# Performance work log

Measured on AMD Instinct MI355X. Metric: run time of the kernel, lower is better.

The kernel has to match this reference:

```python
import jax, jax.numpy as jnp
import numpy as np

B, T, E, H, D, NL = 2, 1024, 2048, 16, 128, 3
MAXL = T * (2 ** (NL - 1))  # k length doubles each layer: T, 2T, 4T


def _rms_norm(x, w, eps=1e-5):
    return x * jax.lax.rsqrt(jnp.mean(x * x, axis=-1, keepdims=True) + eps) * w


def _rope(x, cos, sin):
    # x: [B, S, H, D]; cos/sin: [>=S, D/2]; GPT-NeoX style (non-interleaved)
    S = x.shape[1]
    c = cos[:S][None, :, None, :]
    s = sin[:S][None, :, None, :]
    x1, x2 = jnp.split(x, 2, axis=-1)
    return jnp.concatenate([x1 * c - x2 * s, x1 * s + x2 * c], axis=-1)


def _causal_attn(q, k, v):
    # bottom-right-aligned causal (flash_attn_func causal=True with kv longer than q)
    Tq, L = q.shape[1], k.shape[1]
    scale = 1.0 / np.sqrt(q.shape[-1]).astype(np.float32)
    scores = jnp.einsum('bthd,bshd->bhts', q, k) * scale
    i = jnp.arange(Tq)[:, None]
    j = jnp.arange(L)[None, :]
    mask = j <= i + (L - Tq)
    scores = jnp.where(mask[None, None], scores, -jnp.inf)
    p = jax.nn.softmax(scores, axis=-1)
    return jnp.einsum('bhts,bshd->bthd', p, v)


def setup_inputs() -> dict:
    key = jax.random.key(0)
    ks = jax.random.split(key, 6)
    x = jax.random.normal(ks[0], (B, T, E), dtype=jnp.float32)
    inv_freq = 1.0 / (10000.0 ** (np.arange(0, D, 2, dtype=np.float32) / D))  # [D/2]
    ang = np.arange(MAXL, dtype=np.float32)[:, None] * inv_freq[None, :]      # [MAXL, D/2]
    cos = jnp.asarray(np.cos(ang), dtype=jnp.float32)
    sin = jnp.asarray(np.sin(ang), dtype=jnp.float32)
    wq = jax.random.normal(ks[1], (NL, E, E), dtype=jnp.float32) * 0.02
    wk = jax.random.normal(ks[2], (NL, E, E), dtype=jnp.float32) * 0.02
    wv = jax.random.normal(ks[3], (NL, E, E), dtype=jnp.float32) * 0.02
    ln_w = jnp.ones((NL, E), dtype=jnp.float32)
    lambdas = jnp.zeros((NL,), dtype=jnp.float32)
    w_out = jax.random.normal(ks[4], (E, E), dtype=jnp.float32) * 0.02
    final_ln_w = jnp.ones((E,), dtype=jnp.float32)
    alpha = jnp.ones((1,), dtype=jnp.float32)
    return {'x': x, 'cos': cos, 'sin': sin, 'wq': wq, 'wk': wk, 'wv': wv,
            'ln_w': ln_w, 'lambdas': lambdas, 'w_out': w_out,
            'final_ln_w': final_ln_w, 'alpha': alpha}


def reference(x, cos, sin, wq, wk, wv, ln_w, lambdas, w_out, final_ln_w, alpha):
    bsz, tgt_len, embed_dim = x.shape
    # lambda weights: sigmoid then LayerNorm over the NL scalars (no affine)
    lam = jax.nn.sigmoid(lambdas)
    lam = (lam - jnp.mean(lam)) * jax.lax.rsqrt(jnp.var(lam) + 1e-5)
    acc_k, acc_v = [], []
    total = jnp.zeros_like(x)
    for i in range(NL):  # small fixed layer count
        q = (x @ wq[i].T).reshape(bsz, tgt_len, H, D)
        k = (x @ wk[i].T).reshape(bsz, tgt_len, H, D)
        v = (x @ wv[i].T).reshape(bsz, tgt_len, H, D)
        if i > 0:
            k = jnp.concatenate([k] + acc_k, axis=1)
            v = jnp.concatenate([v] + acc_v, axis=1)
        q = _rope(q, cos, sin)
        k = _rope(k, cos, sin)  # note: cached K gets rotary re-applied, as in source
        attn = _causal_attn(q, k, v).reshape(bsz, tgt_len, embed_dim)
        attn = _rms_norm(attn, ln_w[i])
        total = total + attn * lam[i]
        acc_k.append(k)
        acc_v.append(v)
    out = _rms_norm(total + alpha * x, final_ln_w)
    return out @ w_out.T
```

## Files before the change

kernel.cpp:

```cpp
#include <hip/hip_runtime.h>

typedef unsigned short ushort_t;
typedef __attribute__((ext_vector_type(8))) short bf16x8;
typedef __attribute__((ext_vector_type(4))) short bf16x4;
typedef __attribute__((ext_vector_type(4))) float f32x4;
typedef __attribute__((ext_vector_type(4))) unsigned short u16x4;
typedef __attribute__((ext_vector_type(4))) unsigned int u32x4;

#define DEV __device__ __forceinline__

DEV ushort_t f2bf(float f) {
  union { float f; unsigned int u; } a; a.f = f;
  unsigned int u = a.u;
  unsigned int r = (u + 0x7fffu + ((u >> 16) & 1u)) >> 16;
  return (ushort_t)r;
}
DEV float bf2f(ushort_t b) {
  union { float f; unsigned int u; } a; a.u = ((unsigned int)b) << 16;
  return a.f;
}
DEV void gload_lds16(const void* g, void* l) {
  __builtin_amdgcn_global_load_lds((const __attribute__((address_space(1))) void*)g,
                                   (__attribute__((address_space(3))) void*)l, 16, 0, 0);
}
DEV bf16x4 tr16(const ushort_t* l) {
  unsigned a = (unsigned)(unsigned long long)(const __attribute__((address_space(3))) ushort_t*)l;
  bf16x4 d;
  asm volatile("ds_read_b64_tr_b16 %0, %1" : "=v"(d) : "v"(a));
  return d;
}
DEV bf16x8 ldsb128(const ushort_t* l) {
  unsigned a = (unsigned)(unsigned long long)(const __attribute__((address_space(3))) ushort_t*)l;
  bf16x8 d;
  asm volatile("ds_read_b128 %0, %1" : "=v"(d) : "v"(a));
  return d;
}

__global__ __launch_bounds__(256) void f2b_kernel(const float* __restrict__ in,
                                                  ushort_t* __restrict__ out, int n) {
  int base = (blockIdx.x * 256 + threadIdx.x) * 4;
  if (base >= n) return;
  f32x4 v = *(const f32x4*)(in + base);
  u16x4 o;
  o.x = f2bf(v.x); o.y = f2bf(v.y); o.z = f2bf(v.z); o.w = f2bf(v.w);
  *(u16x4*)(out + base) = o;
}

__global__ __launch_bounds__(256) void f2b3_kernel(const float* __restrict__ a, const float* __restrict__ b,
                                                   const float* __restrict__ c, ushort_t* __restrict__ out) {
  int id = blockIdx.x * 256 + threadIdx.x;
  int sel = id >> 20, k = (id & 1048575) * 4;
  const float* src = sel == 0 ? a : sel == 1 ? b : c;
  f32x4 v = *(const f32x4*)(src + k);
  u16x4 o;
  o.x = f2bf(v.x); o.y = f2bf(v.y); o.z = f2bf(v.z); o.w = f2bf(v.w);
  *(u16x4*)(out + (size_t)sel * 4194304 + k) = o;
}

__global__ void lam_kernel(const float* __restrict__ lambdas, float* __restrict__ lam) {
  if (threadIdx.x == 0 && blockIdx.x == 0) {
    float l0 = 1.f / (1.f + __expf(-lambdas[0]));
    float l1 = 1.f / (1.f + __expf(-lambdas[1]));
    float l2 = 1.f / (1.f + __expf(-lambdas[2]));
    float mean = (l0 + l1 + l2) * (1.f / 3.f);
    float d0 = l0 - mean, d1 = l1 - mean, d2 = l2 - mean;
    float var = (d0 * d0 + d1 * d1 + d2 * d2) * (1.f / 3.f);
    float rs = rsqrtf(var + 1e-5f);
    lam[0] = d0 * rs; lam[1] = d1 * rs; lam[2] = d2 * rs;
  }
}

DEV void gemm_core(const ushort_t* __restrict__ A, const ushort_t* __restrict__ Bm,
                   ushort_t* lsA, ushort_t* lsB, int bm, int bn, f32x4 (&acc)[4][4]) {
  const int K = 2048;
  int tid = threadIdx.x;
  int w = tid >> 6, lane = tid & 63;
  int g = lane >> 4, r = lane & 15;
  int wm = w >> 1, wn = w & 1;
#pragma unroll
  for (int i = 0; i < 4; ++i)
#pragma unroll
    for (int j = 0; j < 4; ++j) acc[i][j] = 0.f;

  for (int kk = 0; kk < K; kk += 32) {
    __syncthreads();
#pragma unroll
    for (int j2 = 0; j2 < 2; ++j2) {
      int eb = w * 1024 + j2 * 512;
      int ebl = eb + lane * 8;
      int rr = ebl >> 5, cc = ebl & 31;
      gload_lds16(A + (size_t)(bm * 128 + rr) * K + kk + cc, lsA + eb);
      gload_lds16(Bm + (size_t)(bn * 128 + rr) * K + kk + cc, lsB + eb);
    }
    __syncthreads();
    bf16x8 af[4], bfr[4];
#pragma unroll
    for (int i = 0; i < 4; ++i)
      af[i] = *(const bf16x8*)(lsA + (wm * 64 + i * 16 + r) * 32 + g * 8);
#pragma unroll
    for (int j = 0; j < 4; ++j)
      bfr[j] = *(const bf16x8*)(lsB + (wn * 64 + j * 16 + r) * 32 + g * 8);
#pragma unroll
    for (int i = 0; i < 4; ++i)
#pragma unroll
      for (int j = 0; j < 4; ++j)
        acc[i][j] = __builtin_amdgcn_mfma_f32_16x16x32_bf16(af[i], bfr[j], acc[i][j], 0, 0, 0);
  }
}

__global__ __launch_bounds__(256) void gemm_qkv(
    const ushort_t* __restrict__ A,
    const ushort_t* __restrict__ Bq, const ushort_t* __restrict__ Bk, const ushort_t* __restrict__ Bv,
    ushort_t* __restrict__ Cq, ushort_t* __restrict__ Ck, ushort_t* __restrict__ Cv, int Lkv) {
  __shared__ __align__(16) ushort_t lsA[4096];
  __shared__ __align__(16) ushort_t lsB[4096];
  int sel = blockIdx.x >> 4, bn = blockIdx.x & 15, bm = blockIdx.y;
  const ushort_t* Bm = (sel == 0) ? Bq : (sel == 1) ? Bk : Bv;
  ushort_t* C = (sel == 0) ? Cq : (sel == 1) ? Ck : Cv;
  int Lsel = (sel == 0) ? 1024 : Lkv;
  f32x4 acc[4][4];
  gemm_core(A, Bm, lsA, lsB, bm, bn, acc);
  int lane = threadIdx.x & 63, w = threadIdx.x >> 6;
  int g = lane >> 4, r = lane & 15, wm = w >> 1, wn = w & 1;
#pragma unroll
  for (int i = 0; i < 4; ++i)
#pragma unroll
    for (int j = 0; j < 4; ++j) {
      int row0 = bm * 128 + wm * 64 + i * 16 + g * 4;
      int col = bn * 128 + wn * 64 + j * 16 + r;
#pragma unroll
      for (int t = 0; t < 4; ++t) {
        int row = row0 + t;
        int b2 = row >> 10, t2 = row & 1023;
        C[(size_t)(b2 * Lsel + t2) * 2048 + col] = f2bf(acc[i][j][t]);
      }
    }
}

__global__ __launch_bounds__(256) void gemm_bt_f32(
    const ushort_t* __restrict__ A, const ushort_t* __restrict__ Bm, float* __restrict__ C) {
  __shared__ __align__(16) ushort_t lsA[4096];
  __shared__ __align__(16) ushort_t lsB[4096];
  int bn = blockIdx.x, bm = blockIdx.y;
  f32x4 acc[4][4];
  gemm_core(A, Bm, lsA, lsB, bm, bn, acc);
  int lane = threadIdx.x & 63, w = threadIdx.x >> 6;
  int g = lane >> 4, r = lane & 15, wm = w >> 1, wn = w & 1;
#pragma unroll
  for (int i = 0; i < 4; ++i)
#pragma unroll
    for (int j = 0; j < 4; ++j) {
      int row0 = bm * 128 + wm * 64 + i * 16 + g * 4;
      int col = bn * 128 + wn * 64 + j * 16 + r;
#pragma unroll
      for (int t = 0; t < 4; ++t)
        C[(size_t)(row0 + t) * 2048 + col] = acc[i][j][t];
    }
}

__global__ __launch_bounds__(256) void rope_seg(const ushort_t* __restrict__ src, ushort_t* __restrict__ dst,
                                                const float* __restrict__ cosT, const float* __restrict__ sinT,
                                                int Ls, int s0, int Ld, int dpos0, int cnt) {
  int bp = blockIdx.x;
  int b = bp / cnt, pidx = bp % cnt;
  int pos = dpos0 + pidx;
  int pi = threadIdx.x * 4;
  int h = pi >> 6, d = pi & 63;
  const ushort_t* s_ = src + ((size_t)(b * Ls + s0 + pidx) * 16 + h) * 128 + d;
  ushort_t* d_ = dst + ((size_t)(b * Ld + pos) * 16 + h) * 128 + d;
  f32x4 c4 = *(const f32x4*)(cosT + (size_t)pos * 64 + d);
  f32x4 s4 = *(const f32x4*)(sinT + (size_t)pos * 64 + d);
  u16x4 x1 = *(const u16x4*)(s_);
  u16x4 x2 = *(const u16x4*)(s_ + 64);
  u16x4 o1, o2;
#pragma unroll
  for (int k = 0; k < 4; ++k) {
    float a = bf2f(x1[k]), bb = bf2f(x2[k]);
    o1[k] = f2bf(a * c4[k] - bb * s4[k]);
    o2[k] = f2bf(a * s4[k] + bb * c4[k]);
  }
  *(u16x4*)d_ = o1;
  *(u16x4*)(d_ + 64) = o2;
}

__global__ __launch_bounds__(256) void copy_seg(const ushort_t* __restrict__ src, ushort_t* __restrict__ dst,
                                                int Ls, int s0, int Ld, int dpos0, int cnt) {
  int bp = blockIdx.x;
  int b = bp / cnt, pidx = bp % cnt;
  const u32x4* s = (const u32x4*)(src + (size_t)(b * Ls + s0 + pidx) * 2048);
  u32x4* d = (u32x4*)(dst + (size_t)(b * Ld + dpos0 + pidx) * 2048);
  d[threadIdx.x] = s[threadIdx.x];
}

__global__ __launch_bounds__(256, 4) void attn_kernel(
    const ushort_t* __restrict__ Q, const ushort_t* __restrict__ Kc, const ushort_t* __restrict__ Vc,
    float* __restrict__ Opart, float2* __restrict__ Ml, int Lk) {
  __shared__ __align__(16) ushort_t lsK[8192];
  __shared__ __align__(16) ushort_t lsV[8192];
  const float sc = 0.08838834764831843f;

  int bid = (int)blockIdx.x;
  int swz = (bid & 7) * 128 + (bid >> 3);
  int s = swz & 1;
  int rest = swz >> 1;

  int w = threadIdx.x >> 6, lane = threadIdx.x & 63;
  int bq = rest & 15, h = (rest >> 4) & 15, b = rest >> 8;
  int qt = bq * 4 + w;
  int g = lane >> 4, r = lane & 15;
  int off = Lk - 1024;

  const ushort_t* qbase = Q + ((size_t)(b * 1024 + qt * 16 + r) * 16 + h) * 128;
  bf16x8 qf[4];
#pragma unroll
  for (int c = 0; c < 4; ++c) qf[c] = *(const bf16x8*)(qbase + c * 32 + g * 8);

  int t = threadIdx.x;
  int krow0 = t >> 4,        kc0 = (t & 15) ^ (krow0 & 7);
  int krow1 = (t + 256) >> 4, kc1 = (t & 15) ^ (krow1 & 7);
  const size_t adv = 32 * 2048;
  const size_t adv2 = 2 * adv;
  const ushort_t* srcK0 = Kc + ((size_t)(b * Lk + krow0) * 16 + h) * 128 + kc0 * 8 + s * adv;
  const ushort_t* srcK1 = Kc + ((size_t)(b * Lk + krow1) * 16 + h) * 128 + kc1 * 8 + s * adv;
  int L0 = t, L1 = t + 256;
  int vrow0 = ((L0 >> 3) & 7) * 4 + ((L0 >> 1) & 3), vd0 = (L0 >> 6) * 16 + (L0 & 1) * 8;
  int vrow1 = ((L1 >> 3) & 7) * 4 + ((L1 >> 1) & 3), vd1 = (L1 >> 6) * 16 + (L1 & 1) * 8;
  const ushort_t* srcV0 = Vc + ((size_t)(b * Lk + vrow0) * 16 + h) * 128 + vd0 + s * adv;
  const ushort_t* srcV1 = Vc + ((size_t)(b * Lk + vrow1) * 16 + h) * 128 + vd1 + s * adv;

  auto STAGE = [&](int buf) {
    ushort_t* k0 = lsK + buf * 4096 + w * 512;
    ushort_t* v0 = lsV + buf * 4096 + w * 512;
    gload_lds16(srcK0, k0);
    gload_lds16(srcK1, k0 + 2048);
    gload_lds16(srcV0, v0);
    gload_lds16(srcV1, v0 + 2048);
    srcK0 += adv2; srcK1 += adv2; srcV0 += adv2; srcV1 += adv2;
  };

  float m_run = -1e30f, l_run = 0.f;
  f32x4 o[8];
#pragma unroll
  for (int c = 0; c < 8; ++c) o[c] = 0.f;

  int qp = qt * 16 + r + off;
  int nkt_w = ((qt * 16 + 15 + off) >> 5) + 1;
  int nkt_blk = (((bq * 4 + 3) * 16 + 15 + off) >> 5) + 1;
  int ntile = (nkt_blk - s + 1) >> 1;

  if (ntile > 0) {
    STAGE(0);
    for (int it = 0; it < ntile; ++it) {
      int kt = s + it * 2;
      int cur = it & 1;
      if (it + 1 < ntile) {
        STAGE(cur ^ 1);
        asm volatile("s_waitcnt vmcnt(4)" ::: "memory");
      } else {
        asm volatile("s_waitcnt vmcnt(0)" ::: "memory");
      }
      __builtin_amdgcn_s_barrier();
      __builtin_amdgcn_sched_barrier(0);
      if (kt < nkt_w) {
        const ushort_t* Kb = lsK + cur * 4096;
        const ushort_t* Vb = lsV + cur * 4096;
        f32x4 st[2];
#pragma unroll
        for (int ks = 0; ks < 2; ++ks) {
          bf16x8 kf[4];
#pragma unroll
          for (int c = 0; c < 4; ++c)
            kf[c] = ldsb128(Kb + (ks * 16 + r) * 128 + ((c * 32 + g * 8) ^ ((r & 7) * 8)));
          asm volatile("s_waitcnt lgkmcnt(0)" ::: "memory");
          __builtin_amdgcn_sched_barrier(0);
          __builtin_amdgcn_s_setprio(1);
          f32x4 acc = 0.f;
#pragma unroll
          for (int c = 0; c < 4; ++c)
            acc = __builtin_amdgcn_mfma_f32_16x16x32_bf16(kf[c], qf[c], acc, 0, 0, 0);
          __builtin_amdgcn_s_setprio(0);
          st[ks] = acc;
        }
        float pmax = -1e30f;
        int kp0 = kt * 32;
#pragma unroll
        for (int ks = 0; ks < 2; ++ks)
#pragma unroll
          for (int j = 0; j < 4; ++j) {
            int key = kp0 + ks * 16 + g * 4 + j;
            float sv = st[ks][j] * sc;
            if (key > qp) sv = -1e30f;
            st[ks][j] = sv;
            pmax = fmaxf(pmax, sv);
          }
        pmax = fmaxf(pmax, __shfl_xor(pmax, 16, 64));
        pmax = fmaxf(pmax, __shfl_xor(pmax, 32, 64));
        if (!__all(pmax <= m_run + 8.f)) {
          float mnew = fmaxf(m_run, pmax);
          float corr = __expf(m_run - mnew);
          l_run *= corr;
#pragma unroll
          for (int c = 0; c < 8; ++c)
#pragma unroll
            for (int tt = 0; tt < 4; ++tt) o[c][tt] *= corr;
          m_run = mnew;
        }
        float psum = 0.f;
        bf16x4 pf[2];
#pragma unroll
        for (int ks = 0; ks < 2; ++ks)
#pragma unroll
          for (int j = 0; j < 4; ++j) {
            float pe = __expf(st[ks][j] - m_run);
            psum += pe;
            pf[ks][j] = (short)f2bf(pe);
          }
        psum += __shfl_xor(psum, 16, 64);
        psum += __shfl_xor(psum, 32, 64);
        l_run += psum;
#pragma unroll
        for (int half = 0; half < 2; ++half) {
          bf16x4 vf[8];
#pragma unroll
          for (int i = 0; i < 8; ++i)
            vf[i] = tr16(Vb + (half * 4 + (i >> 1)) * 512 + (i & 1) * 256);
          asm volatile("s_waitcnt lgkmcnt(0)" ::: "memory");
          __builtin_amdgcn_sched_barrier(0);
          __builtin_amdgcn_s_setprio(1);
#pragma unroll
          for (int db = 0; db < 4; ++db) {
            int dblk = half * 4 + db;
            o[dblk] = __builtin_amdgcn_mfma_f32_16x16x16bf16_1k(vf[db * 2], pf[0], o[dblk], 0, 0, 0);
            o[dblk] = __builtin_amdgcn_mfma_f32_16x16x16bf16_1k(vf[db * 2 + 1], pf[1], o[dblk], 0, 0, 0);
          }
          __builtin_amdgcn_s_setprio(0);
        }
      }
      __builtin_amdgcn_sched_barrier(0);
      __builtin_amdgcn_s_barrier();
    }
  }
  float* ob = Opart + (size_t)s * 4194304 + ((size_t)(b * 1024 + qt * 16 + r) * 16 + h) * 128;
#pragma unroll
  for (int dblk = 0; dblk < 8; ++dblk)
    *(f32x4*)(ob + dblk * 16 + g * 4) = o[dblk];
  if (g == 0) {
    float2 ml; ml.x = m_run; ml.y = l_run;
    Ml[((size_t)(s * 2 + b) * 1024 + qt * 16 + r) * 16 + h] = ml;
  }
}

template <int FIRST>
__global__ __launch_bounds__(256) void rms_combine(const float* __restrict__ Opart, const float2* __restrict__ Ml,
                                                   const float* __restrict__ lnw, const float* __restrict__ lam,
                                                   int li, float* __restrict__ total) {
  int row = blockIdx.x;
  int t8 = threadIdx.x * 8;
  int h = t8 >> 7;
  float2 ml0 = Ml[(size_t)row * 16 + h];
  float2 ml1 = Ml[(size_t)(row + 2048) * 16 + h];
  float M = fmaxf(ml0.x, ml1.x);
  float w0 = __expf(ml0.x - M), w1 = __expf(ml1.x - M);
  float rinv = 1.f / (w0 * ml0.y + w1 * ml1.y);
  w0 *= rinv; w1 *= rinv;
  const float* a0 = Opart + (size_t)row * 2048 + t8;
  const float* a1 = a0 + 4194304;
  f32x4 p00 = *(const f32x4*)(a0);
  f32x4 p01 = *(const f32x4*)(a0 + 4);
  f32x4 p10 = *(const f32x4*)(a1);
  f32x4 p11 = *(const f32x4*)(a1 + 4);
  f32x4 v0, v1;
#pragma unroll
  for (int k = 0; k < 4; ++k) {
    v0[k] = w0 * p00[k] + w1 * p10[k];
    v1[k] = w0 * p01[k] + w1 * p11[k];
  }
  float ss = v0.x * v0.x + v0.y * v0.y + v0.z * v0.z + v0.w * v0.w +
             v1.x * v1.x + v1.y * v1.y + v1.z * v1.z + v1.w * v1.w;
#pragma unroll
  for (int m = 1; m < 64; m <<= 1) ss += __shfl_xor(ss, m, 64);
  __shared__ float red[4];
  int w = threadIdx.x >> 6, lane = threadIdx.x & 63;
  if (lane == 0) red[w] = ss;
  __syncthreads();
  ss = red[0] + red[1] + red[2] + red[3];
  float sca = rsqrtf(ss * (1.f / 2048.f) + 1e-5f) * lam[li];
  f32x4 w0v = *(const f32x4*)(lnw + t8);
  f32x4 w1v = *(const f32x4*)(lnw + t8 + 4);
  float* o = total + (size_t)row * 2048 + t8;
  f32x4 r0, r1;
#pragma unroll
  for (int k = 0; k < 4; ++k) { r0[k] = v0[k] * sca * w0v[k]; r1[k] = v1[k] * sca * w1v[k]; }
  if (!FIRST) {
    f32x4 q0 = *(const f32x4*)(o);
    f32x4 q1 = *(const f32x4*)(o + 4);
#pragma unroll
    for (int k = 0; k < 4; ++k) { r0[k] += q0[k]; r1[k] += q1[k]; }
  }
  *(f32x4*)(o) = r0;
  *(f32x4*)(o + 4) = r1;
}

__global__ __launch_bounds__(256) void final_norm(const float* __restrict__ total, const float* __restrict__ x,
                                                  const float* __restrict__ alphap, const float* __restrict__ flw,
                                                  ushort_t* __restrict__ ybf) {
  int row = blockIdx.x;
  float al = alphap[0];
  int t8 = threadIdx.x * 8;
  const float* tp = total + (size_t)row * 2048 + t8;
  const float* xp = x + (size_t)row * 2048 + t8;
  f32x4 t0 = *(const f32x4*)(tp);
  f32x4 t1 = *(const f32x4*)(tp + 4);
  f32x4 x0 = *(const f32x4*)(xp);
  f32x4 x1 = *(const f32x4*)(xp + 4);
  float y[8];
#pragma unroll
  for (int k = 0; k < 4; ++k) { y[k] = t0[k] + al * x0[k]; y[4 + k] = t1[k] + al * x1[k]; }
  float ss = 0.f;
#pragma unroll
  for (int k = 0; k < 8; ++k) ss += y[k] * y[k];
#pragma unroll
  for (int m = 1; m < 64; m <<= 1) ss += __shfl_xor(ss, m, 64);
  __shared__ float red[4];
  int w = threadIdx.x >> 6, lane = threadIdx.x & 63;
  if (lane == 0) red[w] = ss;
  __syncthreads();
  ss = red[0] + red[1] + red[2] + red[3];
  float s = rsqrtf(ss * (1.f / 2048.f) + 1e-5f);
  f32x4 w0 = *(const f32x4*)(flw + t8);
  f32x4 w1 = *(const f32x4*)(flw + t8 + 4);
  u16x4 o0, o1;
#pragma unroll
  for (int k = 0; k < 4; ++k) {
    o0[k] = f2bf(y[k] * s * w0[k]);
    o1[k] = f2bf(y[4 + k] * s * w1[k]);
  }
  *(u16x4*)(ybf + (size_t)row * 2048 + t8) = o0;
  *(u16x4*)(ybf + (size_t)row * 2048 + t8 + 4) = o1;
}

extern "C" void kernel_launch(void* const* d_in, const int* in_sizes, int n_in,
                              void* d_out, int out_size, void* d_ws, size_t ws_size,
                              hipStream_t stream) {
  const float* x = (const float*)d_in[0];
  const float* cosT = (const float*)d_in[1];
  const float* sinT = (const float*)d_in[2];
  const float* wq = (const float*)d_in[3];
  const float* wk = (const float*)d_in[4];
  const float* wv = (const float*)d_in[5];
  const float* lnw = (const float*)d_in[6];
  const float* lambdas = (const float*)d_in[7];
  const float* w_out = (const float*)d_in[8];
  const float* flw = (const float*)d_in[9];
  const float* alpha = (const float*)d_in[10];

  const size_t ME = 4194304ull;
  char* p = (char*)d_ws;
  size_t off = 0;
  auto alc = [&](size_t bytes) -> void* {
    void* r = p + off;
    off += (bytes + 255) & ~(size_t)255;
    return r;
  };
  ushort_t* xb = (ushort_t*)alc(ME * 2);
  void* uni = alc(2 * ME * 4);
  ushort_t* wl = (ushort_t*)uni;
  float* Opart = (float*)uni;
  ushort_t* q = (ushort_t*)alc(ME * 2);
  ushort_t* K0 = (ushort_t*)alc(ME * 2);
  ushort_t* K1 = (ushort_t*)alc(2 * ME * 2);
  ushort_t* K2 = (ushort_t*)alc(4 * ME * 2);
  ushort_t* V0 = (ushort_t*)alc(ME * 2);
  ushort_t* V1 = (ushort_t*)alc(2 * ME * 2);
  ushort_t* V2 = (ushort_t*)alc(4 * ME * 2);
  float* total = (float*)alc(ME * 4);
  float2* Ml = (float2*)alc(65536 * 8);
  float* lam = (float*)alc(256);
  ushort_t* ybf = q;

  f2b_kernel<<<4096, 256, 0, stream>>>(x, xb, 4194304);
  lam_kernel<<<1, 64, 0, stream>>>(lambdas, lam);

  ushort_t* Kc[3] = {K0, K1, K2};
  ushort_t* Vc[3] = {V0, V1, V2};

  for (int li = 0; li < 3; ++li) {
    int L = 1024 << li;
    size_t woff = (size_t)li * ME;
    f2b3_kernel<<<12288, 256, 0, stream>>>(wq + woff, wk + woff, wv + woff, wl);
    gemm_qkv<<<dim3(48, 16), 256, 0, stream>>>(xb, wl, wl + ME, wl + 2 * ME,
                                               q, Kc[li], Vc[li], L);
    rope_seg<<<2048, 256, 0, stream>>>(q, q, cosT, sinT, 1024, 0, 1024, 0, 1024);
    rope_seg<<<2048, 256, 0, stream>>>(Kc[li], Kc[li], cosT, sinT, L, 0, L, 0, 1024);
    if (li == 1) {
      rope_seg<<<2048, 256, 0, stream>>>(K0, K1, cosT, sinT, 1024, 0, 2048, 1024, 1024);
      copy_seg<<<2048, 256, 0, stream>>>(V0, V1, 1024, 0, 2048, 1024, 1024);
    } else if (li == 2) {
      copy_seg<<<2048, 256, 0, stream>>>(K1, K2, 2048, 1024, 4096, 1024, 1024);
      rope_seg<<<4096, 256, 0, stream>>>(K1, K2, cosT, sinT, 2048, 0, 4096, 2048, 2048);
      copy_seg<<<2048, 256, 0, stream>>>(V1, V2, 2048, 1024, 4096, 1024, 1024);
      copy_seg<<<4096, 256, 0, stream>>>(V1, V2, 2048, 0, 4096, 2048, 2048);
    }
    attn_kernel<<<1024, 256, 0, stream>>>(q, Kc[li], Vc[li], Opart, Ml, L);
    if (li == 0)
      rms_combine<1><<<2048, 256, 0, stream>>>(Opart, Ml, lnw, lam, 0, total);
    else
      rms_combine<0><<<2048, 256, 0, stream>>>(Opart, Ml, lnw + (size_t)li * 2048, lam, li, total);
  }

  f2b_kernel<<<4096, 256, 0, stream>>>(w_out, wl, 4194304);
  final_norm<<<2048, 256, 0, stream>>>(total, x, alpha, flw, ybf);
  gemm_bt_f32<<<dim3(16, 16), 256, 0, stream>>>(ybf, wl, (float*)d_out);
}
```

Before: 595.1 us.

## Fuse rope/copy launches, store attention partials in bf16, split-K the output GEMM

Merges the separate rope and copy launches per layer into single combined kernels, which cuts launch count. Attention split partial outputs are now stored as bf16 instead of fp32, halving the traffic between attn_kernel and rms_combine at some precision cost. The final output GEMM is split over K into two halves (512 blocks instead of 256) to fill more CUs, and an add kernel sums the two fp32 partials. The w_out bf16 copy moves to the K0 buffer so the partials can live in the shared scratch region.

```diff
diff --git a/kernel.cpp b/kernel.cpp
--- a/kernel.cpp
+++ b/kernel.cpp
@@ -71,7 +71,8 @@
 }
 
 DEV void gemm_core(const ushort_t* __restrict__ A, const ushort_t* __restrict__ Bm,
-                   ushort_t* lsA, ushort_t* lsB, int bm, int bn, f32x4 (&acc)[4][4]) {
+                   ushort_t* lsA, ushort_t* lsB, int bm, int bn, int kbeg, int kend,
+                   f32x4 (&acc)[4][4]) {
   const int K = 2048;
   int tid = threadIdx.x;
   int w = tid >> 6, lane = tid & 63;
@@ -82,7 +83,7 @@
 #pragma unroll
     for (int j = 0; j < 4; ++j) acc[i][j] = 0.f;
 
-  for (int kk = 0; kk < K; kk += 32) {
+  for (int kk = kbeg; kk < kend; kk += 32) {
     __syncthreads();
 #pragma unroll
     for (int j2 = 0; j2 < 2; ++j2) {
@@ -119,7 +120,7 @@
   ushort_t* C = (sel == 0) ? Cq : (sel == 1) ? Ck : Cv;
   int Lsel = (sel == 0) ? 1024 : Lkv;
   f32x4 acc[4][4];
-  gemm_core(A, Bm, lsA, lsB, bm, bn, acc);
+  gemm_core(A, Bm, lsA, lsB, bm, bn, 0, 2048, acc);
   int lane = threadIdx.x & 63, w = threadIdx.x >> 6;
   int g = lane >> 4, r = lane & 15, wm = w >> 1, wn = w & 1;
 #pragma unroll
@@ -137,13 +138,14 @@
     }
 }
 
-__global__ __launch_bounds__(256) void gemm_bt_f32(
-    const ushort_t* __restrict__ A, const ushort_t* __restrict__ Bm, float* __restrict__ C) {
+__global__ __launch_bounds__(256) void gemm_bt_part(
+    const ushort_t* __restrict__ A, const ushort_t* __restrict__ Bm, float* __restrict__ P) {
   __shared__ __align__(16) ushort_t lsA[4096];
   __shared__ __align__(16) ushort_t lsB[4096];
-  int bn = blockIdx.x, bm = blockIdx.y;
+  int bn = blockIdx.x, bm = blockIdx.y, s = blockIdx.z;
   f32x4 acc[4][4];
-  gemm_core(A, Bm, lsA, lsB, bm, bn, acc);
+  gemm_core(A, Bm, lsA, lsB, bm, bn, s * 1024, (s + 1) * 1024, acc);
+  float* C = P + (size_t)s * 4194304;
   int lane = threadIdx.x & 63, w = threadIdx.x >> 6;
   int g = lane >> 4, r = lane & 15, wm = w >> 1, wn = w & 1;
 #pragma unroll
@@ -158,10 +160,19 @@
     }
 }
 
-__global__ __launch_bounds__(256) void rope_seg(const ushort_t* __restrict__ src, ushort_t* __restrict__ dst,
-                                                const float* __restrict__ cosT, const float* __restrict__ sinT,
-                                                int Ls, int s0, int Ld, int dpos0, int cnt) {
-  int bp = blockIdx.x;
+__global__ __launch_bounds__(256) void add2_kernel(const float* __restrict__ a, const float* __restrict__ b,
+                                                   float* __restrict__ out) {
+  int i = (blockIdx.x * 256 + threadIdx.x) * 4;
+  f32x4 va = *(const f32x4*)(a + i);
+  f32x4 vb = *(const f32x4*)(b + i);
+  f32x4 r;
+#pragma unroll
+  for (int k = 0; k < 4; ++k) r[k] = va[k] + vb[k];
+  *(f32x4*)(out + i) = r;
+}
+
+DEV void rope_body(const ushort_t* src, ushort_t* dst, const float* cosT, const float* sinT,
+                   int Ls, int s0, int Ld, int dpos0, int cnt, int bp) {
   int b = bp / cnt, pidx = bp % cnt;
   int pos = dpos0 + pidx;
   int pi = threadIdx.x * 4;
@@ -182,19 +193,43 @@
   *(u16x4*)d_ = o1;
   *(u16x4*)(d_ + 64) = o2;
 }
-
-__global__ __launch_bounds__(256) void copy_seg(const ushort_t* __restrict__ src, ushort_t* __restrict__ dst,
-                                                int Ls, int s0, int Ld, int dpos0, int cnt) {
-  int bp = blockIdx.x;
+DEV void copy_body(const ushort_t* src, ushort_t* dst, int Ls, int s0, int Ld, int dpos0,
+                   int cnt, int bp) {
   int b = bp / cnt, pidx = bp % cnt;
   const u32x4* s = (const u32x4*)(src + (size_t)(b * Ls + s0 + pidx) * 2048);
   u32x4* d = (u32x4*)(dst + (size_t)(b * Ld + dpos0 + pidx) * 2048);
   d[threadIdx.x] = s[threadIdx.x];
 }
 
+__global__ __launch_bounds__(256) void rope_qk(ushort_t* q, ushort_t* Kc,
+                                               const float* __restrict__ cosT, const float* __restrict__ sinT,
+                                               int L) {
+  int bp = blockIdx.x;
+  if (bp < 2048) rope_body(q, q, cosT, sinT, 1024, 0, 1024, 0, 1024, bp);
+  else rope_body(Kc, Kc, cosT, sinT, L, 0, L, 0, 1024, bp - 2048);
+}
+
+__global__ __launch_bounds__(256) void layer1_cache(const ushort_t* __restrict__ K0, ushort_t* __restrict__ K1,
+                                                    const ushort_t* __restrict__ V0, ushort_t* __restrict__ V1,
+                                                    const float* __restrict__ cosT, const float* __restrict__ sinT) {
+  int bp = blockIdx.x;
+  if (bp < 2048) rope_body(K0, K1, cosT, sinT, 1024, 0, 2048, 1024, 1024, bp);
+  else copy_body(V0, V1, 1024, 0, 2048, 1024, 1024, bp - 2048);
+}
+
+__global__ __launch_bounds__(256) void layer2_cache(const ushort_t* __restrict__ K1, ushort_t* __restrict__ K2,
+                                                    const ushort_t* __restrict__ V1, ushort_t* __restrict__ V2,
+                                                    const float* __restrict__ cosT, const float* __restrict__ sinT) {
+  int bp = blockIdx.x;
+  if (bp < 2048) copy_body(K1, K2, 2048, 1024, 4096, 1024, 1024, bp);
+  else if (bp < 6144) rope_body(K1, K2, cosT, sinT, 2048, 0, 4096, 2048, 2048, bp - 2048);
+  else if (bp < 8192) copy_body(V1, V2, 2048, 1024, 4096, 1024, 1024, bp - 6144);
+  else copy_body(V1, V2, 2048, 0, 4096, 2048, 2048, bp - 8192);
+}
+
 __global__ __launch_bounds__(256, 4) void attn_kernel(
     const ushort_t* __restrict__ Q, const ushort_t* __restrict__ Kc, const ushort_t* __restrict__ Vc,
-    float* __restrict__ Opart, float2* __restrict__ Ml, int Lk) {
+    ushort_t* __restrict__ Opart, float2* __restrict__ Ml, int Lk) {
   __shared__ __align__(16) ushort_t lsK[8192];
   __shared__ __align__(16) ushort_t lsV[8192];
   const float sc = 0.08838834764831843f;
@@ -340,10 +375,14 @@
       __builtin_amdgcn_s_barrier();
     }
   }
-  float* ob = Opart + (size_t)s * 4194304 + ((size_t)(b * 1024 + qt * 16 + r) * 16 + h) * 128;
-#pragma unroll
-  for (int dblk = 0; dblk < 8; ++dblk)
-    *(f32x4*)(ob + dblk * 16 + g * 4) = o[dblk];
+  ushort_t* ob = Opart + (size_t)s * 4194304 + ((size_t)(b * 1024 + qt * 16 + r) * 16 + h) * 128;
+#pragma unroll
+  for (int dblk = 0; dblk < 8; ++dblk) {
+    u16x4 ov;
+#pragma unroll
+    for (int tt = 0; tt < 4; ++tt) ov[tt] = f2bf(o[dblk][tt]);
+    *(u16x4*)(ob + dblk * 16 + g * 4) = ov;
+  }
   if (g == 0) {
     float2 ml; ml.x = m_run; ml.y = l_run;
     Ml[((size_t)(s * 2 + b) * 1024 + qt * 16 + r) * 16 + h] = ml;
@@ -351,7 +390,7 @@
 }
 
 template <int FIRST>
-__global__ __launch_bounds__(256) void rms_combine(const float* __restrict__ Opart, const float2* __restrict__ Ml,
+__global__ __launch_bounds__(256) void rms_combine(const ushort_t* __restrict__ Opart, const float2* __restrict__ Ml,
                                                    const float* __restrict__ lnw, const float* __restrict__ lam,
                                                    int li, float* __restrict__ total) {
   int row = blockIdx.x;
@@ -363,17 +402,17 @@
   float w0 = __expf(ml0.x - M), w1 = __expf(ml1.x - M);
   float rinv = 1.f / (w0 * ml0.y + w1 * ml1.y);
   w0 *= rinv; w1 *= rinv;
-  const float* a0 = Opart + (size_t)row * 2048 + t8;
-  const float* a1 = a0 + 4194304;
-  f32x4 p00 = *(const f32x4*)(a0);
-  f32x4 p01 = *(const f32x4*)(a0 + 4);
-  f32x4 p10 = *(const f32x4*)(a1);
-  f32x4 p11 = *(const f32x4*)(a1 + 4);
+  const ushort_t* a0 = Opart + (size_t)row * 2048 + t8;
+  const ushort_t* a1 = a0 + 4194304;
+  u16x4 p00 = *(const u16x4*)(a0);
+  u16x4 p01 = *(const u16x4*)(a0 + 4);
+  u16x4 p10 = *(const u16x4*)(a1);
+  u16x4 p11 = *(const u16x4*)(a1 + 4);
   f32x4 v0, v1;
 #pragma unroll
   for (int k = 0; k < 4; ++k) {
-    v0[k] = w0 * p00[k] + w1 * p10[k];
-    v1[k] = w0 * p01[k] + w1 * p11[k];
+    v0[k] = w0 * bf2f(p00[k]) + w1 * bf2f(p10[k]);
+    v1[k] = w0 * bf2f(p01[k]) + w1 * bf2f(p11[k]);
   }
   float ss = v0.x * v0.x + v0.y * v0.y + v0.z * v0.z + v0.w * v0.w +
              v1.x * v1.x + v1.y * v1.y + v1.z * v1.z + v1.w * v1.w;
@@ -465,7 +504,8 @@
   ushort_t* xb = (ushort_t*)alc(ME * 2);
   void* uni = alc(2 * ME * 4);
   ushort_t* wl = (ushort_t*)uni;
-  float* Opart = (float*)uni;
+  ushort_t* Opart = (ushort_t*)uni;
+  float* Ppart = (float*)uni;
   ushort_t* q = (ushort_t*)alc(ME * 2);
   ushort_t* K0 = (ushort_t*)alc(ME * 2);
   ushort_t* K1 = (ushort_t*)alc(2 * ME * 2);
@@ -477,6 +517,7 @@
   float2* Ml = (float2*)alc(65536 * 8);
   float* lam = (float*)alc(256);
   ushort_t* ybf = q;
+  ushort_t* wob = K0;
 
   f2b_kernel<<<4096, 256, 0, stream>>>(x, xb, 4194304);
   lam_kernel<<<1, 64, 0, stream>>>(lambdas, lam);
@@ -490,17 +531,11 @@
     f2b3_kernel<<<12288, 256, 0, stream>>>(wq + woff, wk + woff, wv + woff, wl);
     gemm_qkv<<<dim3(48, 16), 256, 0, stream>>>(xb, wl, wl + ME, wl + 2 * ME,
                                                q, Kc[li], Vc[li], L);
-    rope_seg<<<2048, 256, 0, stream>>>(q, q, cosT, sinT, 1024, 0, 1024, 0, 1024);
-    rope_seg<<<2048, 256, 0, stream>>>(Kc[li], Kc[li], cosT, sinT, L, 0, L, 0, 1024);
-    if (li == 1) {
-      rope_seg<<<2048, 256, 0, stream>>>(K0, K1, cosT, sinT, 1024, 0, 2048, 1024, 1024);
-      copy_seg<<<2048, 256, 0, stream>>>(V0, V1, 1024, 0, 2048, 1024, 1024);
-    } else if (li == 2) {
-      copy_seg<<<2048, 256, 0, stream>>>(K1, K2, 2048, 1024, 4096, 1024, 1024);
-      rope_seg<<<4096, 256, 0, stream>>>(K1, K2, cosT, sinT, 2048, 0, 4096, 2048, 2048);
-      copy_seg<<<2048, 256, 0, stream>>>(V1, V2, 2048, 1024, 4096, 1024, 1024);
-      copy_seg<<<4096, 256, 0, stream>>>(V1, V2, 2048, 0, 4096, 2048, 2048);
-    }
+    rope_qk<<<4096, 256, 0, stream>>>(q, Kc[li], cosT, sinT, L);
+    if (li == 1)
+      layer1_cache<<<4096, 256, 0, stream>>>(K0, K1, V0, V1, cosT, sinT);
+    else if (li == 2)
+      layer2_cache<<<12288, 256, 0, stream>>>(K1, K2, V1, V2, cosT, sinT);
     attn_kernel<<<1024, 256, 0, stream>>>(q, Kc[li], Vc[li], Opart, Ml, L);
     if (li == 0)
       rms_combine<1><<<2048, 256, 0, stream>>>(Opart, Ml, lnw, lam, 0, total);
@@ -508,7 +543,8 @@
       rms_combine<0><<<2048, 256, 0, stream>>>(Opart, Ml, lnw + (size_t)li * 2048, lam, li, total);
   }
 
-  f2b_kernel<<<4096, 256, 0, stream>>>(w_out, wl, 4194304);
+  f2b_kernel<<<4096, 256, 0, stream>>>(w_out, wob, 4194304);
   final_norm<<<2048, 256, 0, stream>>>(total, x, alpha, flw, ybf);
-  gemm_bt_f32<<<dim3(16, 16), 256, 0, stream>>>(ybf, wl, (float*)d_out);
-}
+  gemm_bt_part<<<dim3(16, 16, 2), 256, 0, stream>>>(ybf, wob, Ppart);
+  add2_kernel<<<4096, 256, 0, stream>>>(Ppart, Ppart + ME, (float*)d_out);
+}
```

New measurement: 580.3 us. 1.03x faster.
